# Optimization experiments

Measured on AMD Instinct MI355X. Metric: run time of the kernel, lower is better.

Reference implementation:

```python
import jax, jax.numpy as jnp
import numpy as np

NUM_HEADS = 16
WINDOW = 256


def setup_inputs() -> dict:
    key = jax.random.key(0)
    ks = jax.random.split(key, 4)
    B, S, D = 1, 4096, 1024
    scale = 1.0 / np.sqrt(D)  # keep logits sane with random weights
    x = jax.random.normal(ks[0], (B, S, D), dtype=jnp.float32)
    Wq = jax.random.normal(ks[1], (D, D), dtype=jnp.float32) * scale
    Wk = jax.random.normal(ks[2], (D, D), dtype=jnp.float32) * scale
    Wv = jax.random.normal(ks[3], (D, D), dtype=jnp.float32) * scale
    bq = jnp.zeros((D,), dtype=jnp.float32)
    bk = jnp.zeros((D,), dtype=jnp.float32)
    bv = jnp.zeros((D,), dtype=jnp.float32)
    return {"x": x, "Wq": Wq, "bq": bq, "Wk": Wk, "bk": bk, "Wv": Wv, "bv": bv}


def reference(x, Wq, bq, Wk, bk, Wv, bv):
    B, S, D = x.shape
    H = NUM_HEADS
    depth = D // H

    def split_heads(t):
        return t.reshape(B, S, H, depth).transpose(0, 2, 1, 3)  # [B,H,S,depth]

    # torch nn.Linear: y = x @ W.T + b
    Q = split_heads(x @ Wq.T + bq)
    K = split_heads(x @ Wk.T + bk)
    V = split_heads(x @ Wv.T + bv)

    scores = jnp.einsum("bhqd,bhkd->bhqk", Q, K) / jnp.sqrt(jnp.float32(depth))
    idx = jnp.arange(S)
    band = jnp.abs(idx[None, :] - idx[:, None]) <= WINDOW  # [S,S] local window
    scores = jnp.where(band[None, None], scores, -jnp.inf)
    attn = jax.nn.softmax(scores, axis=-1)
    out = jnp.einsum("bhqk,bhkd->bhqd", attn, V)
    return out.transpose(0, 2, 1, 3).reshape(B, S, D)
```

## Files before the change

### kernel.cpp

```cpp
#include <hip/hip_runtime.h>
#include <hip/hip_bf16.h>

typedef __attribute__((ext_vector_type(4))) float f32x4;
typedef __attribute__((ext_vector_type(16))) float f32x16;
typedef __attribute__((ext_vector_type(8))) short s16x8;
typedef __attribute__((ext_vector_type(4))) float float4_t;
typedef __attribute__((ext_vector_type(2))) unsigned int u32x2;

union U8 { s16x8 v; unsigned u[4]; };

__device__ __forceinline__ ushort f2bf(float f) {
  union { float f; unsigned u; } v; v.f = f;
  unsigned r = v.u + 0x7fffu + ((v.u >> 16) & 1u);
  return (ushort)(r >> 16);
}

__device__ __forceinline__ void async_copy16(ushort* lds, const ushort* g) {
  __builtin_amdgcn_global_load_lds(
      (const __attribute__((address_space(1))) unsigned int*)g,
      (__attribute__((address_space(3))) unsigned int*)lds, 16, 0, 0);
}

__device__ __forceinline__ unsigned lds_addr(const void* p) {
  return (unsigned)(unsigned long long)(__attribute__((address_space(3))) const void*)p;
}

#define TRRD(dst, addr, off_lit) \
  asm volatile("ds_read_b64_tr_b16 %0, %1 offset:" #off_lit : "=v"(dst) : "v"(addr))

__global__ __launch_bounds__(256) void convert_kernel(
    const float* __restrict__ x, const float* __restrict__ Wq,
    const float* __restrict__ Wk, const float* __restrict__ Wv,
    ushort* __restrict__ xs, ushort* __restrict__ ws) {
  int b = blockIdx.x;
  if (b < 2048) {
    int c = b * 256 + threadIdx.x;
    int kc = c & 127;
    int m = c >> 7;
    const float4_t* s = (const float4_t*)&x[(size_t)m * 1024 + kc * 8];
    float4_t a0 = s[0], a1 = s[1];
    s16x8 v;
    v[0] = (short)f2bf(a0[0]); v[1] = (short)f2bf(a0[1]);
    v[2] = (short)f2bf(a0[2]); v[3] = (short)f2bf(a0[3]);
    v[4] = (short)f2bf(a1[0]); v[5] = (short)f2bf(a1[1]);
    v[6] = (short)f2bf(a1[2]); v[7] = (short)f2bf(a1[3]);
    int tm = m >> 7, tk = kc >> 3, r = m & 127, c8 = kc & 7;
    *(s16x8*)&xs[((size_t)(tm * 16 + tk) * 128 + r) * 64 + ((c8 ^ (r & 7)) * 8)] = v;
  } else {
    int c = (b - 2048) * 256 + threadIdx.x;
    int kc = c & 127;
    int n = c >> 7;
    int p = n >> 10, nW = n & 1023;
    const float* __restrict__ W = (p == 0) ? Wq : (p == 1) ? Wk : Wv;
    const float4_t* s = (const float4_t*)&W[(size_t)nW * 1024 + kc * 8];
    float4_t a0 = s[0], a1 = s[1];
    s16x8 v;
    v[0] = (short)f2bf(a0[0]); v[1] = (short)f2bf(a0[1]);
    v[2] = (short)f2bf(a0[2]); v[3] = (short)f2bf(a0[3]);
    v[4] = (short)f2bf(a1[0]); v[5] = (short)f2bf(a1[1]);
    v[6] = (short)f2bf(a1[2]); v[7] = (short)f2bf(a1[3]);
    unsigned tn3 = (unsigned)n / 192u;
    unsigned r = (unsigned)n - tn3 * 192u;
    int tk = kc >> 3, c8 = kc & 7;
    *(s16x8*)&ws[((size_t)(tn3 * 16 + tk) * 192 + r) * 64 + ((c8 ^ (r & 7)) * 8)] = v;
  }
}

__global__ __launch_bounds__(512, 2) void qkv_gemm_kernel(
    const ushort* __restrict__ xs, const ushort* __restrict__ wsb,
    const float* __restrict__ bq, const float* __restrict__ bk,
    const float* __restrict__ bv, ushort* __restrict__ qkv) {
  __shared__ ushort lA[2][16384];
  __shared__ ushort lB[2][12288];
  const int t = threadIdx.x;
  const int lane = t & 63, w = t >> 6;
  const int wm = w >> 1, wn = w & 1;
  const int l15 = lane & 15, l4 = lane >> 4;
  const int phys = blockIdx.x;
  const int swz = (phys & 7) * 32 + (phys >> 3);
  const int xcd = swz >> 5, jj = swz & 31;
  const int bm = (xcd >> 1) * 4 + (jj >> 3);
  const int bn = (xcd & 1) * 8 + (jj & 7);

  const ushort* Apan = xs + (size_t)(2 * bm) * 16 * 8192;
  const ushort* Bpan = wsb + (size_t)bn * 16 * 12288;

  f32x4 acc[4][6];
#pragma unroll
  for (int i = 0; i < 4; i++)
#pragma unroll
    for (int j = 0; j < 6; j++) acc[i][j] = (f32x4)0.f;

#define STAGE_A(buf, kt)                                                        \
  do {                                                                          \
    const ushort* s0 = Apan + (size_t)(kt) * 8192;                              \
    const ushort* s1 = Apan + (size_t)(16 + (kt)) * 8192;                       \
    async_copy16(&lA[buf][t * 8], s0 + t * 8);                                  \
    async_copy16(&lA[buf][(t + 512) * 8], s0 + (t + 512) * 8);                  \
    async_copy16(&lA[buf][8192 + t * 8], s1 + t * 8);                           \
    async_copy16(&lA[buf][8192 + (t + 512) * 8], s1 + (t + 512) * 8);           \
  } while (0)
#define STAGE_B(buf, kt)                                                        \
  do {                                                                          \
    const ushort* s2 = Bpan + (size_t)(kt) * 12288;                             \
    async_copy16(&lB[buf][t * 8], s2 + t * 8);                                  \
    async_copy16(&lB[buf][(t + 512) * 8], s2 + (t + 512) * 8);                  \
    async_copy16(&lB[buf][(t + 1024) * 8], s2 + (t + 1024) * 8);                \
  } while (0)

  STAGE_A(0, 0);
  STAGE_B(0, 0);
  asm volatile("s_waitcnt vmcnt(0)");
  __builtin_amdgcn_s_barrier();

  for (int kt = 0; kt < 16; ++kt) {
    const int cur = kt & 1;
    s16x8 af[4], bfr[6];
#pragma unroll
    for (int mi = 0; mi < 4; mi++) {
      int ra = wm * 64 + mi * 16 + l15;
      int g = l4 ^ (ra & 7);
      af[mi] = *(const s16x8*)&lA[cur][ra * 64 + g * 8];
    }
#pragma unroll
    for (int ni = 0; ni < 6; ni++) {
      int rb = wn * 96 + ni * 16 + l15;
      int g = l4 ^ (rb & 7);
      bfr[ni] = *(const s16x8*)&lB[cur][rb * 64 + g * 8];
    }
    if (kt + 1 < 16) STAGE_A(cur ^ 1, kt + 1);
    asm volatile("s_waitcnt lgkmcnt(0)");
    __builtin_amdgcn_sched_barrier(0);
    __builtin_amdgcn_s_setprio(1);
#pragma unroll
    for (int mi = 0; mi < 4; mi++)
#pragma unroll
      for (int ni = 0; ni < 6; ni++)
        acc[mi][ni] = __builtin_amdgcn_mfma_f32_16x16x32_bf16(af[mi], bfr[ni], acc[mi][ni], 0, 0, 0);
    __builtin_amdgcn_s_setprio(0);
#pragma unroll
    for (int mi = 0; mi < 4; mi++) {
      int ra = wm * 64 + mi * 16 + l15;
      int g = (4 + l4) ^ (ra & 7);
      af[mi] = *(const s16x8*)&lA[cur][ra * 64 + g * 8];
    }
#pragma unroll
    for (int ni = 0; ni < 6; ni++) {
      int rb = wn * 96 + ni * 16 + l15;
      int g = (4 + l4) ^ (rb & 7);
      bfr[ni] = *(const s16x8*)&lB[cur][rb * 64 + g * 8];
    }
    if (kt + 1 < 16) STAGE_B(cur ^ 1, kt + 1);
    asm volatile("s_waitcnt lgkmcnt(0)");
    __builtin_amdgcn_sched_barrier(0);
    __builtin_amdgcn_s_setprio(1);
#pragma unroll
    for (int mi = 0; mi < 4; mi++)
#pragma unroll
      for (int ni = 0; ni < 6; ni++)
        acc[mi][ni] = __builtin_amdgcn_mfma_f32_16x16x32_bf16(af[mi], bfr[ni], acc[mi][ni], 0, 0, 0);
    __builtin_amdgcn_s_setprio(0);
    asm volatile("s_waitcnt vmcnt(0)");
    __builtin_amdgcn_s_barrier();
  }
#undef STAGE_A
#undef STAGE_B

#pragma unroll
  for (int ni = 0; ni < 6; ni++) {
    int col = bn * 192 + wn * 96 + ni * 16 + l15;
    int p = col >> 10;
    const float* bias = (p == 0) ? bq : (p == 1) ? bk : bv;
    float b = bias[col & 1023];
    float qscale = (p == 0) ? 0.125f * 1.44269504f : 1.0f;
    int h = (col >> 6) & 15, dd = col & 63;
    size_t base = ((size_t)(p * 16 + h) * 4096) * 64 + dd;
#pragma unroll
    for (int mi = 0; mi < 4; mi++) {
#pragma unroll
      for (int r = 0; r < 4; r++) {
        int s = bm * 256 + wm * 64 + mi * 16 + l4 * 4 + r;
        float v = (acc[mi][ni][r] + b) * qscale;
        qkv[base + (size_t)s * 64] = f2bf(v);
      }
    }
  }
}

__global__ __launch_bounds__(256) void attn_local_kernel(
    const ushort* __restrict__ qkv, float* __restrict__ out) {
  __shared__ ushort lds[2][2][4096];
  const int bid = blockIdx.x;
  const int wid = (bid & 7) * 64 + (bid >> 3);
  const int hd = wid >> 5;
  const int q0 = (wid & 31) << 7;
  const int t = threadIdx.x;
  const int lane = t & 63, w = t >> 6;
  const int l15 = lane & 15, l31 = lane & 31;
  const int b4 = (lane >> 4) & 1, hf = lane >> 5;
  const int qw = q0 + w * 32;
  const int myq = qw + l31;

  const ushort* __restrict__ Q = qkv;
  const ushort* __restrict__ K = qkv + (size_t)16 * 4096 * 64;
  const ushort* __restrict__ V = K + (size_t)16 * 4096 * 64;

  s16x8 qf[4];
  {
    const ushort* qp = &Q[((size_t)hd * 4096 + myq) * 64];
#pragma unroll
    for (int kc = 0; kc < 4; kc++) qf[kc] = *(const s16x8*)&qp[16 * kc + 8 * hf];
  }

  U8 ones;
  {
    unsigned w1 = (l31 == 0) ? 0x3F803F80u : 0u;
    ones.u[0] = w1; ones.u[1] = w1; ones.u[2] = w1; ones.u[3] = w1;
  }

  f32x16 oa0 = (f32x16)0.f, oa1 = (f32x16)0.f, oden = (f32x16)0.f;
  float mrow = -1e30f;

  const unsigned vtr0 = lds_addr(&lds[0][1][0]) +
      (unsigned)(hf * 1024 + (l15 >> 2) * 128 + b4 * 32 + (l15 & 3) * 8);

  int kstart = q0 - 256; if (kstart < 0) kstart = 0;
  int kend = q0 + 384; if (kend > 4096) kend = 4096;

#define STAGE_KV(buf, kb)                                                      \
  do {                                                                         \
    const ushort* Kg = &K[((size_t)hd * 4096 + (kb)) * 64];                    \
    const ushort* Vg = &V[((size_t)hd * 4096 + (kb)) * 64];                    \
    _Pragma("unroll") for (int i = 0; i < 2; i++) {                            \
      int off = i * 2048 + t * 8;                                              \
      int row = off >> 6;                                                      \
      int c8s = (off >> 3) & 7;                                                \
      async_copy16(&lds[buf][0][off], &Kg[row * 64 + ((c8s ^ (row & 7)) * 8)]);\
      async_copy16(&lds[buf][1][off], &Vg[off]);                               \
    }                                                                          \
  } while (0)

  STAGE_KV(0, kstart);
  asm volatile("s_waitcnt vmcnt(0)");
  __builtin_amdgcn_s_barrier();

  for (int kb = kstart; kb < kend; kb += 64) {
    const int cur = ((kb - kstart) >> 6) & 1;
    if (kb + 64 < kend) {
      if (cur) STAGE_KV(0, kb + 64); else STAGE_KV(1, kb + 64);
    }
    bool active = (kb + 63 >= qw - 256) && (kb <= qw + 31 + 256);
    if (active) {
      const ushort* lK = &lds[cur][0][0];
      f32x16 st0 = (f32x16)0.f, st1 = (f32x16)0.f;
      __builtin_amdgcn_s_setprio(1);
#pragma unroll
      for (int kc = 0; kc < 4; kc++) {
        int c8 = 2 * kc + hf;
        int r0 = l31;
        s16x8 kf0 = *(const s16x8*)&lK[r0 * 64 + ((c8 ^ (r0 & 7)) * 8)];
        st0 = __builtin_amdgcn_mfma_f32_32x32x16_bf16(kf0, qf[kc], st0, 0, 0, 0);
        int r1 = 32 + l31;
        s16x8 kf1 = *(const s16x8*)&lK[r1 * 64 + ((c8 ^ (r1 & 7)) * 8)];
        st1 = __builtin_amdgcn_mfma_f32_32x32x16_bf16(kf1, qf[kc], st1, 0, 0, 0);
      }
      __builtin_amdgcn_s_setprio(0);
      const bool interior = (kb >= qw - 225) && (kb <= qw + 193);
      if (!interior) {
        int base0 = myq - kb - 4 * hf + 256;
#pragma unroll
        for (int r = 0; r < 16; r++) {
          int ko = (r & 3) + 8 * (r >> 2);
          if (!((unsigned)(base0 - ko) <= 512u)) st0[r] = -3e38f;
          if (!((unsigned)(base0 - 32 - ko) <= 512u)) st1[r] = -3e38f;
        }
      }
      float rm;
      {
        float a = fmaxf(fmaxf(st0[0], st0[1]), fmaxf(st0[2], st0[3]));
        float b = fmaxf(fmaxf(st0[4], st0[5]), fmaxf(st0[6], st0[7]));
        float c = fmaxf(fmaxf(st0[8], st0[9]), fmaxf(st0[10], st0[11]));
        float d = fmaxf(fmaxf(st0[12], st0[13]), fmaxf(st0[14], st0[15]));
        float e = fmaxf(fmaxf(st1[0], st1[1]), fmaxf(st1[2], st1[3]));
        float f = fmaxf(fmaxf(st1[4], st1[5]), fmaxf(st1[6], st1[7]));
        float g = fmaxf(fmaxf(st1[8], st1[9]), fmaxf(st1[10], st1[11]));
        float h2 = fmaxf(fmaxf(st1[12], st1[13]), fmaxf(st1[14], st1[15]));
        rm = fmaxf(fmaxf(fmaxf(a, b), fmaxf(c, d)), fmaxf(fmaxf(e, f), fmaxf(g, h2)));
      }
      rm = fmaxf(rm, __shfl_xor(rm, 32));
      if (__any(rm > mrow + 8.0f)) {
        float mn = fmaxf(mrow, rm);
        float sc = __builtin_amdgcn_exp2f(mrow - mn);
        mrow = mn;
        int srcB = (lane & 32); srcB += srcB >> 3;
#pragma unroll
        for (int r = 0; r < 16; r++) {
          float scr = __shfl(sc, srcB + (r & 3) + 8 * (r >> 2));
          oa0[r] *= scr; oa1[r] *= scr; oden[r] *= scr;
        }
      }
      const unsigned vtr = vtr0 + (unsigned)cur * 16384u;
      u32x2 v0, v1, v2, v3, v4, v5, v6, v7, v8, v9, v10, v11, v12, v13, v14, v15;
      TRRD(v0, vtr, 0);     TRRD(v1, vtr, 512);  TRRD(v2, vtr, 64);    TRRD(v3, vtr, 576);
      TRRD(v4, vtr, 2048);  TRRD(v5, vtr, 2560); TRRD(v6, vtr, 2112);  TRRD(v7, vtr, 2624);
      TRRD(v8, vtr, 4096);  TRRD(v9, vtr, 4608); TRRD(v10, vtr, 4160); TRRD(v11, vtr, 4672);
      TRRD(v12, vtr, 6144); TRRD(v13, vtr, 6656); TRRD(v14, vtr, 6208); TRRD(v15, vtr, 6720);
      U8 pa0, pa1, pa2, pa3;
#define PACK(STV, RB, OUT)                                                     \
  do {                                                                         \
    float e0 = __builtin_amdgcn_exp2f(STV[RB + 0] - mrow);                     \
    float e1 = __builtin_amdgcn_exp2f(STV[RB + 1] - mrow);                     \
    float e2 = __builtin_amdgcn_exp2f(STV[RB + 2] - mrow);                     \
    float e3 = __builtin_amdgcn_exp2f(STV[RB + 3] - mrow);                     \
    float e4 = __builtin_amdgcn_exp2f(STV[RB + 4] - mrow);                     \
    float e5 = __builtin_amdgcn_exp2f(STV[RB + 5] - mrow);                     \
    float e6 = __builtin_amdgcn_exp2f(STV[RB + 6] - mrow);                     \
    float e7 = __builtin_amdgcn_exp2f(STV[RB + 7] - mrow);                     \
    unsigned a0, a1, b0, b1;                                                   \
    asm("v_cvt_pk_bf16_f32 %0, %1, %2" : "=v"(a0) : "v"(e0), "v"(e1));         \
    asm("v_cvt_pk_bf16_f32 %0, %1, %2" : "=v"(a1) : "v"(e2), "v"(e3));         \
    asm("v_cvt_pk_bf16_f32 %0, %1, %2" : "=v"(b0) : "v"(e4), "v"(e5));         \
    asm("v_cvt_pk_bf16_f32 %0, %1, %2" : "=v"(b1) : "v"(e6), "v"(e7));         \
    asm volatile("v_permlane32_swap_b32 %0, %1" : "+v"(a0), "+v"(b0));         \
    asm volatile("v_permlane32_swap_b32 %0, %1" : "+v"(a1), "+v"(b1));         \
    OUT.u[0] = a0; OUT.u[1] = a1; OUT.u[2] = b0; OUT.u[3] = b1;                \
  } while (0)
      PACK(st0, 0, pa0); PACK(st0, 8, pa1); PACK(st1, 0, pa2); PACK(st1, 8, pa3);
#undef PACK
#define MFMA3(PA, VA0, VA1, VB0, VB1)                                          \
  do {                                                                         \
    U8 f0, f1;                                                                 \
    f0.u[0] = VA0[0]; f0.u[1] = VA0[1]; f0.u[2] = VA1[0]; f0.u[3] = VA1[1];    \
    f1.u[0] = VB0[0]; f1.u[1] = VB0[1]; f1.u[2] = VB1[0]; f1.u[3] = VB1[1];    \
    __builtin_amdgcn_s_setprio(1);                                             \
    oa0 = __builtin_amdgcn_mfma_f32_32x32x16_bf16(PA.v, f0.v, oa0, 0, 0, 0);   \
    oa1 = __builtin_amdgcn_mfma_f32_32x32x16_bf16(PA.v, f1.v, oa1, 0, 0, 0);   \
    oden = __builtin_amdgcn_mfma_f32_32x32x16_bf16(PA.v, ones.v, oden, 0, 0, 0);\
    __builtin_amdgcn_s_setprio(0);                                             \
  } while (0)
      asm volatile("s_waitcnt lgkmcnt(12)");
      __builtin_amdgcn_sched_barrier(0);
      MFMA3(pa0, v0, v1, v2, v3);
      asm volatile("s_waitcnt lgkmcnt(8)");
      __builtin_amdgcn_sched_barrier(0);
      MFMA3(pa1, v4, v5, v6, v7);
      asm volatile("s_waitcnt lgkmcnt(4)");
      __builtin_amdgcn_sched_barrier(0);
      MFMA3(pa2, v8, v9, v10, v11);
      asm volatile("s_waitcnt lgkmcnt(0)");
      __builtin_amdgcn_sched_barrier(0);
      MFMA3(pa3, v12, v13, v14, v15);
#undef MFMA3
    }
    asm volatile("s_waitcnt vmcnt(0)");
    __builtin_amdgcn_s_barrier();
  }
#undef STAGE_KV
#pragma unroll
  for (int r = 0; r < 16; r++) {
    float den = __shfl(oden[r], lane & 32);
    float linv = 1.0f / den;
    int s = qw + (r & 3) + 8 * (r >> 2) + 4 * hf;
    out[(size_t)s * 1024 + hd * 64 + l31] = oa0[r] * linv;
    out[(size_t)s * 1024 + hd * 64 + 32 + l31] = oa1[r] * linv;
  }
}

extern "C" void kernel_launch(void* const* d_in, const int* in_sizes, int n_in,
                              void* d_out, int out_size, void* d_ws, size_t ws_size,
                              hipStream_t stream) {
  const float* x  = (const float*)d_in[0];
  const float* Wq = (const float*)d_in[1];
  const float* bq = (const float*)d_in[2];
  const float* Wk = (const float*)d_in[3];
  const float* bk = (const float*)d_in[4];
  const float* Wv = (const float*)d_in[5];
  const float* bv = (const float*)d_in[6];

  ushort* qkv = (ushort*)d_ws;
  ushort* xs  = (ushort*)((char*)d_ws + (size_t)25165824);
  ushort* wsb = xs + (size_t)4096 * 1024;
  float* out = (float*)d_out;

  convert_kernel<<<3584, 256, 0, stream>>>(x, Wq, Wk, Wv, xs, wsb);
  qkv_gemm_kernel<<<256, 512, 0, stream>>>(xs, wsb, bq, bk, bv, qkv);
  attn_local_kernel<<<512, 256, 0, stream>>>(qkv, out);
}
```

Before: 63.59 us.

## Load GEMM B fragments straight from global into registers, bypassing LDS

After: 92.07 us. 44.8% more time.

```diff
diff --git a/kernel.cpp b/kernel.cpp
--- a/kernel.cpp
+++ b/kernel.cpp
@@ -31,7 +31,7 @@
 __global__ __launch_bounds__(256) void convert_kernel(
     const float* __restrict__ x, const float* __restrict__ Wq,
     const float* __restrict__ Wk, const float* __restrict__ Wv,
-    ushort* __restrict__ xs, ushort* __restrict__ ws) {
+    ushort* __restrict__ xs, ushort* __restrict__ wb) {
   int b = blockIdx.x;
   if (b < 2048) {
     int c = b * 256 + threadIdx.x;
@@ -50,28 +50,24 @@
     int c = (b - 2048) * 256 + threadIdx.x;
     int kc = c & 127;
     int n = c >> 7;
-    int p = n >> 10, nW = n & 1023;
+    int p = n >> 10;
     const float* __restrict__ W = (p == 0) ? Wq : (p == 1) ? Wk : Wv;
-    const float4_t* s = (const float4_t*)&W[(size_t)nW * 1024 + kc * 8];
+    const float4_t* s = (const float4_t*)&W[(size_t)(n & 1023) * 1024 + kc * 8];
     float4_t a0 = s[0], a1 = s[1];
     s16x8 v;
     v[0] = (short)f2bf(a0[0]); v[1] = (short)f2bf(a0[1]);
     v[2] = (short)f2bf(a0[2]); v[3] = (short)f2bf(a0[3]);
     v[4] = (short)f2bf(a1[0]); v[5] = (short)f2bf(a1[1]);
     v[6] = (short)f2bf(a1[2]); v[7] = (short)f2bf(a1[3]);
-    unsigned tn3 = (unsigned)n / 192u;
-    unsigned r = (unsigned)n - tn3 * 192u;
-    int tk = kc >> 3, c8 = kc & 7;
-    *(s16x8*)&ws[((size_t)(tn3 * 16 + tk) * 192 + r) * 64 + ((c8 ^ (r & 7)) * 8)] = v;
+    *(s16x8*)&wb[(size_t)n * 1024 + kc * 8] = v;
   }
 }
 
 __global__ __launch_bounds__(512, 2) void qkv_gemm_kernel(
-    const ushort* __restrict__ xs, const ushort* __restrict__ wsb,
+    const ushort* __restrict__ xs, const ushort* __restrict__ wb,
     const float* __restrict__ bq, const float* __restrict__ bk,
     const float* __restrict__ bv, ushort* __restrict__ qkv) {
   __shared__ ushort lA[2][16384];
-  __shared__ ushort lB[2][12288];
   const int t = threadIdx.x;
   const int lane = t & 63, w = t >> 6;
   const int wm = w >> 1, wn = w & 1;
@@ -83,7 +79,7 @@
   const int bn = (xcd & 1) * 8 + (jj & 7);
 
   const ushort* Apan = xs + (size_t)(2 * bm) * 16 * 8192;
-  const ushort* Bpan = wsb + (size_t)bn * 16 * 12288;
+  const ushort* Bb = wb + (size_t)(bn * 192 + wn * 96 + l15) * 1024 + l4 * 8;
 
   f32x4 acc[4][6];
 #pragma unroll
@@ -100,71 +96,56 @@
     async_copy16(&lA[buf][8192 + t * 8], s1 + t * 8);                           \
     async_copy16(&lA[buf][8192 + (t + 512) * 8], s1 + (t + 512) * 8);           \
   } while (0)
-#define STAGE_B(buf, kt)                                                        \
-  do {                                                                          \
-    const ushort* s2 = Bpan + (size_t)(kt) * 12288;                             \
-    async_copy16(&lB[buf][t * 8], s2 + t * 8);                                  \
-    async_copy16(&lB[buf][(t + 512) * 8], s2 + (t + 512) * 8);                  \
-    async_copy16(&lB[buf][(t + 1024) * 8], s2 + (t + 1024) * 8);                \
-  } while (0)
-
+
+  s16x8 B0[6], B1[6];
   STAGE_A(0, 0);
-  STAGE_B(0, 0);
-  asm volatile("s_waitcnt vmcnt(0)");
+#pragma unroll
+  for (int ni = 0; ni < 6; ni++)
+    B0[ni] = *(const s16x8*)&Bb[(size_t)ni * 16384];
+  asm volatile("s_waitcnt vmcnt(6)" ::: "memory");
   __builtin_amdgcn_s_barrier();
 
   for (int kt = 0; kt < 16; ++kt) {
     const int cur = kt & 1;
-    s16x8 af[4], bfr[6];
+    s16x8 a0[4], a1[4];
 #pragma unroll
     for (int mi = 0; mi < 4; mi++) {
       int ra = wm * 64 + mi * 16 + l15;
-      int g = l4 ^ (ra & 7);
-      af[mi] = *(const s16x8*)&lA[cur][ra * 64 + g * 8];
-    }
-#pragma unroll
-    for (int ni = 0; ni < 6; ni++) {
-      int rb = wn * 96 + ni * 16 + l15;
-      int g = l4 ^ (rb & 7);
-      bfr[ni] = *(const s16x8*)&lB[cur][rb * 64 + g * 8];
-    }
+      a0[mi] = *(const s16x8*)&lA[cur][ra * 64 + (l4 ^ (ra & 7)) * 8];
+    }
+#pragma unroll
+    for (int ni = 0; ni < 6; ni++)
+      B1[ni] = *(const s16x8*)&Bb[(size_t)ni * 16384 + kt * 64 + 32];
     if (kt + 1 < 16) STAGE_A(cur ^ 1, kt + 1);
-    asm volatile("s_waitcnt lgkmcnt(0)");
     __builtin_amdgcn_sched_barrier(0);
     __builtin_amdgcn_s_setprio(1);
 #pragma unroll
     for (int mi = 0; mi < 4; mi++)
 #pragma unroll
       for (int ni = 0; ni < 6; ni++)
-        acc[mi][ni] = __builtin_amdgcn_mfma_f32_16x16x32_bf16(af[mi], bfr[ni], acc[mi][ni], 0, 0, 0);
+        acc[mi][ni] = __builtin_amdgcn_mfma_f32_16x16x32_bf16(a0[mi], B0[ni], acc[mi][ni], 0, 0, 0);
     __builtin_amdgcn_s_setprio(0);
 #pragma unroll
     for (int mi = 0; mi < 4; mi++) {
       int ra = wm * 64 + mi * 16 + l15;
-      int g = (4 + l4) ^ (ra & 7);
-      af[mi] = *(const s16x8*)&lA[cur][ra * 64 + g * 8];
-    }
-#pragma unroll
-    for (int ni = 0; ni < 6; ni++) {
-      int rb = wn * 96 + ni * 16 + l15;
-      int g = (4 + l4) ^ (rb & 7);
-      bfr[ni] = *(const s16x8*)&lB[cur][rb * 64 + g * 8];
-    }
-    if (kt + 1 < 16) STAGE_B(cur ^ 1, kt + 1);
-    asm volatile("s_waitcnt lgkmcnt(0)");
-    __builtin_amdgcn_sched_barrier(0);
+      a1[mi] = *(const s16x8*)&lA[cur][ra * 64 + ((4 + l4) ^ (ra & 7)) * 8];
+    }
+    if (kt + 1 < 16) {
+#pragma unroll
+      for (int ni = 0; ni < 6; ni++)
+        B0[ni] = *(const s16x8*)&Bb[(size_t)ni * 16384 + (kt + 1) * 64];
+    }
     __builtin_amdgcn_s_setprio(1);
 #pragma unroll
     for (int mi = 0; mi < 4; mi++)
 #pragma unroll
       for (int ni = 0; ni < 6; ni++)
-        acc[mi][ni] = __builtin_amdgcn_mfma_f32_16x16x32_bf16(af[mi], bfr[ni], acc[mi][ni], 0, 0, 0);
+        acc[mi][ni] = __builtin_amdgcn_mfma_f32_16x16x32_bf16(a1[mi], B1[ni], acc[mi][ni], 0, 0, 0);
     __builtin_amdgcn_s_setprio(0);
-    asm volatile("s_waitcnt vmcnt(0)");
+    asm volatile("s_waitcnt vmcnt(6)" ::: "memory");
     __builtin_amdgcn_s_barrier();
   }
 #undef STAGE_A
-#undef STAGE_B
 
 #pragma unroll
   for (int ni = 0; ni < 6; ni++) {
@@ -379,10 +360,10 @@
 
   ushort* qkv = (ushort*)d_ws;
   ushort* xs  = (ushort*)((char*)d_ws + (size_t)25165824);
-  ushort* wsb = xs + (size_t)4096 * 1024;
+  ushort* wbb = xs + (size_t)4096 * 1024;
   float* out = (float*)d_out;
 
-  convert_kernel<<<3584, 256, 0, stream>>>(x, Wq, Wk, Wv, xs, wsb);
-  qkv_gemm_kernel<<<256, 512, 0, stream>>>(xs, wsb, bq, bk, bv, qkv);
+  convert_kernel<<<3584, 256, 0, stream>>>(x, Wq, Wk, Wv, xs, wbb);
+  qkv_gemm_kernel<<<256, 512, 0, stream>>>(xs, wbb, bq, bk, bv, qkv);
   attn_local_kernel<<<512, 256, 0, stream>>>(qkv, out);
 }
```
